# Kernel optimization log

Hardware: AMD Instinct MI355X
Metric: run time of the kernel (lower is better)

## Reference

```python
import jax, jax.numpy as jnp
import numpy as np

N, E, QL, HID = 1024, 8192, 8, 1024
NH, NKV, HD = 16, 8, 64          # heads, kv heads, head_dim; groups = NH // NKV = 2
INTER = 4096
THETA = 10000.0
EPS = 1e-6


def rmsnorm(x, w):
    v = x.astype(jnp.float32)
    v = v * jax.lax.rsqrt(jnp.mean(v * v, axis=-1, keepdims=True) + EPS)
    return w * v.astype(x.dtype)


def rotate_half(x):
    h = x.shape[-1] // 2
    return jnp.concatenate([-x[..., h:], x[..., :h]], axis=-1)


def rope_tables(seq_len):
    inv_freq = 1.0 / (THETA ** (jnp.arange(0, HD, 2, dtype=jnp.float32) / HD))
    freqs = jnp.arange(seq_len, dtype=jnp.float32)[:, None] * inv_freq[None, :]
    emb = jnp.concatenate([freqs, freqs], axis=-1)  # [seq_len, HD]
    return jnp.cos(emb), jnp.sin(emb)


def setup_inputs() -> dict:
    key = jax.random.key(0)
    ks = jax.random.split(key, 14)
    w = lambda k, sh: (jax.random.normal(k, sh, jnp.float32) * 0.02)
    return {
        "hidden_states": jax.random.normal(ks[0], (N, QL, HID), jnp.float32),
        "edge_index": jax.random.randint(ks[1], (2, E), 0, N, dtype=jnp.int32),
        "edge_hidden_states": jax.random.normal(ks[2], (E, QL, HID), jnp.float32),
        "Wq": w(ks[3], (NH * HD, HID)),
        "Wk": w(ks[4], (NKV * HD, HID)),
        "Wv": w(ks[5], (NKV * HD, HID)),
        "Wo": w(ks[6], (HID, HID)),
        "Wgate": w(ks[7], (INTER, HID)),
        "Wup": w(ks[8], (INTER, HID)),
        "Wdown": w(ks[9], (HID, INTER)),
        "ln1_w": jnp.ones((HID,), jnp.float32),
        "ln2_w": jnp.ones((HID,), jnp.float32),
    }


def gofa_layer(hidden_states, edge_index, edge_hidden_states, Wq, Wk, Wv, Wo,
               Wgate, Wup, Wdown, ln1_w, ln2_w):
    src, dst = edge_index[0], edge_index[1]  # message flows src -> dst
    residual = hidden_states
    x = rmsnorm(hidden_states, ln1_w)  # [N, QL, HID]

    q = x @ Wq.T                     # [N, QL, NH*HD]
    k = x @ Wk.T                     # [N, QL, NKV*HD]
    v = x @ Wv.T
    ek = edge_hidden_states @ Wk.T   # [E, QL, NKV*HD]
    ev = edge_hidden_states @ Wv.T

    # per-edge gather
    q_i = q[dst]                     # [E, QL, NH*HD]
    k_j, v_j = k[src], v[src]        # [E, QL, NKV*HD]

    # interleave node/edge tokens: [E, 2*QL, NKV*HD]
    keys = jnp.stack([k_j, ek], axis=2).reshape(E, 2 * QL, NKV * HD)
    vals = jnp.stack([v_j, ev], axis=2).reshape(E, 2 * QL, NKV * HD)

    qh = q_i.reshape(E, QL, NH, HD).transpose(0, 2, 1, 3)        # [E, NH, QL, HD]
    kh = keys.reshape(E, 2 * QL, NKV, HD).transpose(0, 2, 1, 3)  # [E, NKV, 2QL, HD]
    vh = vals.reshape(E, 2 * QL, NKV, HD).transpose(0, 2, 1, 3)

    cos_k, sin_k = rope_tables(2 * QL)
    cos_q, sin_q = cos_k[:QL], sin_k[:QL]
    qh = qh * cos_q[None, None] + rotate_half(qh) * sin_q[None, None]
    kh = kh * cos_k[None, None] + rotate_half(kh) * sin_k[None, None]

    groups = NH // NKV
    kh = jnp.repeat(kh, groups, axis=1)  # [E, NH, 2QL, HD]
    vh = jnp.repeat(vh, groups, axis=1)

    logits = jnp.einsum('ehqd,ehkd->ehqk', qh, kh) / np.sqrt(HD)  # [E, NH, QL, 2QL]

    # segment softmax over (edges into same dst node) x (2QL key positions)
    seg = jnp.repeat(dst, 2 * QL)                                  # [E*2QL]
    a = logits.transpose(0, 3, 1, 2).reshape(E * 2 * QL, NH, QL)   # [E*2QL, NH, QL]
    m = jax.ops.segment_max(a, seg, num_segments=N)                # [N, NH, QL]
    ex = jnp.exp(a - m[seg])
    s = jax.ops.segment_sum(ex, seg, num_segments=N)
    alpha = ex / (s[seg] + 1e-16)
    alpha = alpha.reshape(E, 2 * QL, NH, QL).transpose(0, 2, 3, 1)  # [E, NH, QL, 2QL]

    out_e = jnp.einsum('ehqk,ehkd->ehqd', alpha, vh)               # [E, NH, QL, HD]
    out_e = out_e.transpose(0, 2, 1, 3).reshape(E, QL, HID)

    agg = jax.ops.segment_sum(out_e, dst, num_segments=N)          # [N, QL, HID]
    attn_out = agg @ Wo.T

    h = residual + attn_out
    h2 = rmsnorm(h, ln2_w)
    mlp = (jax.nn.silu(h2 @ Wgate.T) * (h2 @ Wup.T)) @ Wdown.T
    return h + mlp


def reference(hidden_states, edge_index, edge_hidden_states, Wq, Wk, Wv, Wo,
              Wgate, Wup, Wdown, ln1_w, ln2_w):
    return gofa_layer(hidden_states, edge_index, edge_hidden_states, Wq, Wk, Wv,
                      Wo, Wgate, Wup, Wdown, ln1_w, ln2_w)
```

## Files before the change

### kernel.cpp

```cpp
#include <hip/hip_runtime.h>
#include <cstddef>
#include <cstdint>

constexpr int kN    = 1024;
constexpr int kE    = 8192;
constexpr int kQL   = 8;
constexpr int kHID  = 1024;

typedef __bf16 bf16x8 __attribute__((ext_vector_type(8)));
typedef float  f32x4  __attribute__((ext_vector_type(4)));
typedef unsigned short ushort8 __attribute__((ext_vector_type(8)));

__device__ __forceinline__ unsigned short f2bf(float f) {
  unsigned u = __float_as_uint(f);
  unsigned r = (u + 0x7FFFu + ((u >> 16) & 1u)) >> 16;
  return (unsigned short)r;
}
__device__ __forceinline__ float bf2f(unsigned short u) {
  return __uint_as_float((unsigned)u << 16);
}
__device__ __forceinline__ unsigned pkbf(float a, float b) {
  return (unsigned)f2bf(a) | ((unsigned)f2bf(b) << 16);
}
__device__ __forceinline__ void gload_lds16(const void* g, void* l) {
  __builtin_amdgcn_global_load_lds(
      (const __attribute__((address_space(1))) void*)g,
      (__attribute__((address_space(3))) void*)l, 16, 0, 0);
}

__global__ void rope_tables_kernel(float* __restrict__ ct, float* __restrict__ st) {
  int i = threadIdx.x;
  int p = i >> 5, j = i & 31;
  float inv = expf(-((float)(2 * j) / 64.0f) * logf(10000.0f));
  float ang = (float)p * inv;
  ct[i] = cosf(ang);
  st[i] = sinf(ang);
}

__global__ __launch_bounds__(256) void cvt_kernel(
    const float* __restrict__ in, unsigned short* __restrict__ out, int n8) {
  int i = blockIdx.x * 256 + threadIdx.x;
  if (i >= n8) return;
  const float4* p = (const float4*)(in + (size_t)i * 8);
  float4 a = p[0], b = p[1];
  uint4 o;
  o.x = f2bf(a.x) | ((unsigned)f2bf(a.y) << 16);
  o.y = f2bf(a.z) | ((unsigned)f2bf(a.w) << 16);
  o.z = f2bf(b.x) | ((unsigned)f2bf(b.y) << 16);
  o.w = f2bf(b.z) | ((unsigned)f2bf(b.w) << 16);
  *(uint4*)(out + (size_t)i * 8) = o;
}

__global__ __launch_bounds__(256) void cvt_gu_kernel(
    const float* __restrict__ Wg, const float* __restrict__ Wu,
    unsigned short* __restrict__ out) {
  int i = blockIdx.x * 256 + threadIdx.x;
  int n = i >> 7, ck = (i & 127) * 8;
  int isUp = (n >> 4) & 1;
  int srow = (n >> 6) * 32 + ((n >> 5) & 1) * 16 + (n & 15);
  const float* src = (isUp ? Wu : Wg) + (size_t)srow * 1024 + ck;
  const float4* p = (const float4*)src;
  float4 a = p[0], b = p[1];
  uint4 o;
  o.x = f2bf(a.x) | ((unsigned)f2bf(a.y) << 16);
  o.y = f2bf(a.z) | ((unsigned)f2bf(a.w) << 16);
  o.z = f2bf(b.x) | ((unsigned)f2bf(b.y) << 16);
  o.w = f2bf(b.z) | ((unsigned)f2bf(b.w) << 16);
  *(uint4*)(out + (size_t)n * 1024 + ck) = o;
}

__global__ __launch_bounds__(256) void rmsnorm_bf16_kernel(
    const float* __restrict__ in, const float* __restrict__ w,
    unsigned short* __restrict__ out) {
  __shared__ float red[4];
  int row = blockIdx.x, tid = threadIdx.x;
  const float* p = in + (size_t)row * kHID + tid * 4;
  float4 v = *(const float4*)p;
  float ss = v.x*v.x + v.y*v.y + v.z*v.z + v.w*v.w;
  #pragma unroll
  for (int off = 32; off > 0; off >>= 1) ss += __shfl_down(ss, off);
  int lane = tid & 63, wv = tid >> 6;
  if (lane == 0) red[wv] = ss;
  __syncthreads();
  float tot = red[0] + red[1] + red[2] + red[3];
  float rn = rsqrtf(tot * (1.0f / (float)kHID) + 1e-6f);
  float4 w4 = *(const float4*)(w + tid * 4);
  uint2 o;
  o.x = f2bf(v.x*rn*w4.x) | ((unsigned)f2bf(v.y*rn*w4.y) << 16);
  o.y = f2bf(v.z*rn*w4.z) | ((unsigned)f2bf(v.w*rn*w4.w) << 16);
  *(uint2*)(out + (size_t)row * kHID + tid * 4) = o;
}

template<int OUTMODE, int TM>
__global__ __launch_bounds__(512, 4) void gemmk(
    const unsigned short* __restrict__ A, const unsigned short* __restrict__ B,
    const float* __restrict__ resid, void* __restrict__ Cout,
    const float* __restrict__ ct, const float* __restrict__ st,
    int M, int N, int K) {
  constexpr int ABUFE = TM * 32;
  constexpr int BBUFE = 128 * 32;
  constexpr int WRS   = TM / 4;
  constexpr int MI    = WRS / 16;
  constexpr int LPS   = (TM == 256) ? 3 : 2;
  __shared__ unsigned short As[3 * ABUFE];
  __shared__ unsigned short Bs[3 * BBUFE];
  const int tid = threadIdx.x;
  const int lane = tid & 63, wid = tid >> 6;
  const int gx = gridDim.x;
  int id = blockIdx.y * gx + blockIdx.x;
  {
    const int nwg = gx * gridDim.y;
    const int cpx = nwg >> 3;
    id = (id & 7) * cpx + (id >> 3);
  }
  const int m0 = (id / gx) * TM, n0 = (id % gx) * 128;
  const int wr = wid >> 1, wc = wid & 1;
  const int l15 = lane & 15, lg = lane >> 4;
  const int NT = K >> 5;

  const int sr4 = lane >> 2, sc = lane & 3;
  const int arow0 = (TM == 256) ? (wid * 32 + sr4) : (wid * 16 + sr4);
  const int brow0 = wid * 16 + sr4;
  const unsigned short* Asrc = A + (size_t)(m0 + arow0) * K + (sc ^ ((arow0 >> 1) & 3)) * 8;
  const unsigned short* Bsrc = B + (size_t)(n0 + brow0) * K + (sc ^ ((brow0 >> 1) & 3)) * 8;
  const size_t rK16 = (size_t)16 * K;

#define STAGE(t_, b_) do {                                                   \
    const size_t _k0 = (size_t)(t_) * 32;                                    \
    if (TM == 256) {                                                         \
      gload_lds16(Asrc + _k0,        As + (b_) * ABUFE + wid * 1024);        \
      gload_lds16(Asrc + rK16 + _k0, As + (b_) * ABUFE + wid * 1024 + 512);  \
    } else {                                                                 \
      gload_lds16(Asrc + _k0,        As + (b_) * ABUFE + wid * 512);         \
    }                                                                        \
    gload_lds16(Bsrc + _k0,          Bs + (b_) * BBUFE + wid * 512);         \
  } while (0)

  f32x4 acc[MI][4] = {};
  STAGE(0, 0); STAGE(1, 1);

  const int rck = (lg ^ ((l15 >> 1) & 3)) * 8;
  int cur = 0, nx2 = 2;
  for (int t = 0; t < NT; ++t) {
    __builtin_amdgcn_sched_barrier(0);
    if (t + 1 < NT) asm volatile("s_waitcnt vmcnt(%0)" :: "i"(LPS) : "memory");
    else            asm volatile("s_waitcnt vmcnt(0)" ::: "memory");
    __builtin_amdgcn_s_barrier();
    __builtin_amdgcn_sched_barrier(0);
    if (t + 2 < NT) STAGE(t + 2, nx2);

    const unsigned short* Ab = As + cur * ABUFE + (wr * WRS + l15) * 32 + rck;
    const unsigned short* Bb = Bs + cur * BBUFE + (wc * 64 + l15) * 32 + rck;
    bf16x8 af[MI], bf[4];
    #pragma unroll
    for (int mi = 0; mi < MI; ++mi) af[mi] = *(const bf16x8*)(Ab + mi * 512);
    #pragma unroll
    for (int nj = 0; nj < 4; ++nj) bf[nj] = *(const bf16x8*)(Bb + nj * 512);
    __builtin_amdgcn_s_setprio(1);
    #pragma unroll
    for (int mi = 0; mi < MI; ++mi)
      #pragma unroll
      for (int nj = 0; nj < 4; ++nj)
        acc[mi][nj] = __builtin_amdgcn_mfma_f32_16x16x32_bf16(af[mi], bf[nj], acc[mi][nj], 0, 0, 0);
    __builtin_amdgcn_s_setprio(0);
    cur = (cur == 2) ? 0 : cur + 1;
    nx2 = (nx2 == 2) ? 0 : nx2 + 1;
  }
#undef STAGE

  const int r0 = lg * 4;
  const int bc = n0 + wc * 64;
  #pragma unroll
  for (int mi = 0; mi < MI; ++mi) {
    #pragma unroll
    for (int r = 0; r < 4; ++r) {
      const size_t grow = (size_t)(m0 + wr * WRS + mi * 16 + r0 + r);
      if (OUTMODE == 0) {
        #pragma unroll
        for (int nj = 0; nj < 4; ++nj) {
          const size_t gi = grow * N + (bc + nj * 16 + l15);
          float v = acc[mi][nj][r];
          if (resid) v += resid[gi];
          ((float*)Cout)[gi] = v;
        }
      } else if (OUTMODE == 2) {
        #pragma unroll
        for (int p = 0; p < 2; ++p) {
          float gv = acc[mi][2 * p][r], uv = acc[mi][2 * p + 1][r];
          float res = gv / (1.f + __expf(-gv)) * uv;
          ((unsigned short*)Cout)[grow * (size_t)(N >> 1) + (bc >> 1) + p * 16 + l15] = f2bf(res);
        }
      } else {
        bool doR = false; int pos = 0;
        if (OUTMODE == 3) { doR = bc < 512; pos = 2 * ((int)grow & 7) + 1; }
        if (OUTMODE == 4) {
          if (bc < 1024)      { doR = true; pos = (int)grow & 7; }
          else if (bc < 1536) { doR = true; pos = 2 * ((int)grow & 7); }
        }
        unsigned short* o16 = (unsigned short*)Cout;
        if (doR) {
          #pragma unroll
          for (int nj = 0; nj < 2; ++nj) {
            float a = acc[mi][nj][r], b = acc[mi][nj + 2][r];
            float c = ct[pos * 32 + nj * 16 + l15];
            float s = st[pos * 32 + nj * 16 + l15];
            o16[grow * N + bc + nj * 16 + l15]       = f2bf(a * c - b * s);
            o16[grow * N + bc + (nj + 2) * 16 + l15] = f2bf(b * c + a * s);
          }
        } else {
          #pragma unroll
          for (int nj = 0; nj < 4; ++nj)
            o16[grow * N + bc + nj * 16 + l15] = f2bf(acc[mi][nj][r]);
        }
      }
    }
  }
}

__global__ void csr_count_kernel(const int* __restrict__ dst, int* __restrict__ cnt) {
  int e = blockIdx.x * 256 + threadIdx.x;
  if (e < kE) atomicAdd(&cnt[dst[e]], 1);
}
__global__ __launch_bounds__(1024) void csr_scan_kernel(
    const int* __restrict__ cnt, int* __restrict__ start) {
  __shared__ int tmp[1024];
  int t = threadIdx.x;
  tmp[t] = cnt[t];
  __syncthreads();
  for (int off = 1; off < 1024; off <<= 1) {
    int add = (t >= off) ? tmp[t - off] : 0;
    __syncthreads();
    tmp[t] += add;
    __syncthreads();
  }
  start[t + 1] = tmp[t];
  if (t == 0) start[0] = 0;
}
__global__ void csr_scatter_kernel(const int* __restrict__ dst, const int* __restrict__ start,
                                   int* __restrict__ cursor, int* __restrict__ elist) {
  int e = blockIdx.x * 256 + threadIdx.x;
  if (e < kE) {
    int d = dst[e];
    int pos = atomicAdd(&cursor[d], 1);
    elist[start[d] + pos] = e;
  }
}

__global__ __launch_bounds__(256) void attn_mfma_kernel(
    const unsigned short* __restrict__ qkv,
    const unsigned short* __restrict__ ekv,
    const int* __restrict__ srcIdx, const int* __restrict__ elist,
    const int* __restrict__ start,
    unsigned short* __restrict__ aggb) {
  const int n = blockIdx.x >> 1;
  const int g = (blockIdx.x & 1) * 4 + (threadIdx.x >> 6);
  const int lane = threadIdx.x & 63;
  const int l15 = lane & 15, lg = lane >> 4;

  const int h = g * 2 + (l15 >> 3), q = l15 & 7;
  const unsigned short* qrow = qkv + ((size_t)n * 8 + q) * 2048 + h * 64 + lg * 8;
  const bf16x8 qf0 = *(const bf16x8*)qrow;
  const bf16x8 qf1 = *(const bf16x8*)(qrow + 32);

  float m = -3.4e38f, sh = 0.f;
  f32x4 oacc[4];
  #pragma unroll
  for (int t = 0; t < 4; ++t) oacc[t] = (f32x4){0.f, 0.f, 0.f, 0.f};

  const int kparity = l15 & 1;
  const int t_ = l15 >> 1;
  const int lgh = lg & 1;
  const int eS = lg >> 1;

  const int s0 = start[n], s1 = start[n + 1];
  for (int jj = s0; jj < s1; jj += 2) {
    const int e0 = elist[jj];
    const bool has1 = (jj + 1 < s1);
    const int e1 = has1 ? elist[jj + 1] : e0;
    const int sn0 = srcIdx[e0], sn1 = srcIdx[e1];

    const unsigned short* kr0 = kparity
        ? ekv + ((size_t)e0 * 8 + t_) * 1024 + g * 64 + lg * 8
        : qkv + ((size_t)sn0 * 8 + t_) * 2048 + 1024 + g * 64 + lg * 8;
    const unsigned short* kr1 = kparity
        ? ekv + ((size_t)e1 * 8 + t_) * 1024 + g * 64 + lg * 8
        : qkv + ((size_t)sn1 * 8 + t_) * 2048 + 1024 + g * 64 + lg * 8;
    bf16x8 ka0 = *(const bf16x8*)kr0, ka1 = *(const bf16x8*)(kr0 + 32);
    bf16x8 kc0 = *(const bf16x8*)kr1, kc1 = *(const bf16x8*)(kr1 + 32);

    const int evsel = eS ? e1 : e0;
    const int snsel = eS ? sn1 : sn0;
    const unsigned short* vn = qkv + ((size_t)snsel * 8 + lgh * 4) * 2048 + 1536 + g * 64;
    const unsigned short* ve = ekv + ((size_t)evsel * 8 + lgh * 4) * 1024 + 512 + g * 64;

    f32x4 z = (f32x4){0.f, 0.f, 0.f, 0.f};
    f32x4 sa = __builtin_amdgcn_mfma_f32_16x16x32_bf16(ka0, qf0, z, 0, 0, 0);
    sa       = __builtin_amdgcn_mfma_f32_16x16x32_bf16(ka1, qf1, sa, 0, 0, 0);
    f32x4 sb = __builtin_amdgcn_mfma_f32_16x16x32_bf16(kc0, qf0, z, 0, 0, 0);
    sb       = __builtin_amdgcn_mfma_f32_16x16x32_bf16(kc1, qf1, sb, 0, 0, 0);

    float l0[4], l1[4];
    float lmax = -3.4e38f;
    #pragma unroll
    for (int r = 0; r < 4; ++r) {
      l0[r] = sa[r] * 0.125f;
      l1[r] = has1 ? sb[r] * 0.125f : -3.4e38f;
      lmax = fmaxf(lmax, fmaxf(l0[r], l1[r]));
    }
    lmax = fmaxf(lmax, __shfl_xor(lmax, 16));
    lmax = fmaxf(lmax, __shfl_xor(lmax, 32));
    const float mnew = fmaxf(m, lmax);
    const float scale = __expf(m - mnew);
    float p0[4], p1[4], ps = 0.f;
    #pragma unroll
    for (int r = 0; r < 4; ++r) {
      p0[r] = __expf(l0[r] - mnew);
      p1[r] = __expf(l1[r] - mnew);
      ps += p0[r] + p1[r];
    }
    ps += __shfl_xor(ps, 16);
    ps += __shfl_xor(ps, 32);
    sh = sh * scale + ps;
    m = mnew;

    #pragma unroll
    for (int r = 0; r < 4; ++r) {
      float sr = __shfl(scale, lg * 4 + r);
      #pragma unroll
      for (int t = 0; t < 4; ++t) oacc[t][r] *= sr;
    }

    unsigned w00 = pkbf(p0[0], p0[1]), w01 = pkbf(p0[2], p0[3]);
    unsigned w10 = pkbf(p1[0], p1[1]), w11 = pkbf(p1[2], p1[3]);
    const int L1 = l15 + 32 * lgh, L2 = L1 + 16;
    unsigned a0 = __shfl(w00, L1), a1 = __shfl(w01, L1);
    unsigned a2 = __shfl(w00, L2), a3 = __shfl(w01, L2);
    unsigned b0 = __shfl(w10, L1), b1 = __shfl(w11, L1);
    unsigned b2 = __shfl(w10, L2), b3 = __shfl(w11, L2);
    uint4 wv;
    wv.x = eS ? b0 : a0; wv.y = eS ? b1 : a1;
    wv.z = eS ? b2 : a2; wv.w = eS ? b3 : a3;
    const bf16x8 pf = __builtin_bit_cast(bf16x8, wv);

    #pragma unroll
    for (int t = 0; t < 4; ++t) {
      const int col = t * 16 + l15;
      ushort8 vr;
      #pragma unroll
      for (int j = 0; j < 8; ++j)
        vr[j] = (j & 1) ? ve[(j >> 1) * 1024 + col] : vn[(j >> 1) * 2048 + col];
      const bf16x8 vf = __builtin_bit_cast(bf16x8, vr);
      oacc[t] = __builtin_amdgcn_mfma_f32_16x16x32_bf16(pf, vf, oacc[t], 0, 0, 0);
    }
  }

  #pragma unroll
  for (int r = 0; r < 4; ++r) {
    const float sr = __shfl(sh, lg * 4 + r);
    const float inv = 1.f / (sr + 1e-16f);
    const int hq = lg * 4 + r;
    const int hh = g * 2 + (hq >> 3), qq = hq & 7;
    unsigned short* op = aggb + ((size_t)n * 8 + qq) * 1024 + hh * 64 + l15;
    #pragma unroll
    for (int t = 0; t < 4; ++t) op[t * 16] = f2bf(oacc[t][r] * inv);
  }
}

extern "C" void kernel_launch(void* const* d_in, const int* in_sizes, int n_in,
                              void* d_out, int out_size, void* d_ws, size_t ws_size,
                              hipStream_t stream) {
  const float* hidden = (const float*)d_in[0];
  const int*   eidx   = (const int*)d_in[1];
  const float* ehid   = (const float*)d_in[2];
  const float* Wq     = (const float*)d_in[3];
  const float* Wk     = (const float*)d_in[4];
  const float* Wv     = (const float*)d_in[5];
  const float* Wo     = (const float*)d_in[6];
  const float* Wgate  = (const float*)d_in[7];
  const float* Wup    = (const float*)d_in[8];
  const float* Wdown  = (const float*)d_in[9];
  const float* ln1    = (const float*)d_in[10];
  const float* ln2    = (const float*)d_in[11];
  const int* srcIdx = eidx;
  const int* dstIdx = eidx + kE;

  char* wsb = (char*)d_ws;
  size_t off = 0;
  auto alloc = [&](size_t bytes) { char* p = wsb + off; off += (bytes + 255) & ~(size_t)255; return p; };
  unsigned short* eh16   = (unsigned short*)alloc(134217728);
  unsigned short* ekv16  = (unsigned short*)alloc(134217728);
  unsigned short* qkv16  = (unsigned short*)alloc(33554432);
  unsigned short* x16    = (unsigned short*)alloc(16777216);
  unsigned short* agg16  = (unsigned short*)alloc(16777216);
  float*          hbuf   = (float*)alloc(33554432);
  unsigned short* wqkv16 = (unsigned short*)alloc(4194304);
  unsigned short* wo16   = (unsigned short*)alloc(2097152);
  unsigned short* wgu16  = (unsigned short*)alloc(16777216);
  unsigned short* wd16   = (unsigned short*)alloc(8388608);
  int* cnt    = (int*)alloc(4096);
  int* cursor = (int*)alloc(4096);
  int* startb = (int*)alloc(4352);
  int* elist  = (int*)alloc(32768);
  float* ct   = (float*)alloc(2048);
  float* st   = (float*)alloc(2048);
  unsigned short* gm16 = ekv16;
  unsigned short* h216 = x16;
  float* outp = (float*)d_out;

  hipMemsetAsync(cnt, 0, 8192, stream);
  rope_tables_kernel<<<1, 512, 0, stream>>>(ct, st);

  cvt_kernel<<<32768, 256, 0, stream>>>(ehid,  eh16, 8388608);
  cvt_kernel<<<512,   256, 0, stream>>>(Wq,    wqkv16,                 131072);
  cvt_kernel<<<256,   256, 0, stream>>>(Wk,    wqkv16 + 1024 * 1024,   65536);
  cvt_kernel<<<256,   256, 0, stream>>>(Wv,    wqkv16 + 1536 * 1024,   65536);
  cvt_kernel<<<512,   256, 0, stream>>>(Wo,    wo16,                  131072);
  cvt_gu_kernel<<<4096, 256, 0, stream>>>(Wgate, Wup, wgu16);
  cvt_kernel<<<2048,  256, 0, stream>>>(Wdown, wd16,                  524288);

  csr_count_kernel<<<32, 256, 0, stream>>>(dstIdx, cnt);
  csr_scan_kernel<<<1, 1024, 0, stream>>>(cnt, startb);
  csr_scatter_kernel<<<32, 256, 0, stream>>>(dstIdx, startb, cursor, elist);

  rmsnorm_bf16_kernel<<<kN * kQL, 256, 0, stream>>>(hidden, ln1, x16);

  gemmk<4, 256><<<dim3(16, 32),  512, 0, stream>>>(x16,  wqkv16, nullptr, qkv16, ct, st, 8192, 2048, 1024);
  gemmk<3, 256><<<dim3(8, 256), 512, 0, stream>>>(eh16, wqkv16 + 1024 * 1024, nullptr, ekv16, ct, st, 65536, 1024, 1024);

  attn_mfma_kernel<<<2048, 256, 0, stream>>>(qkv16, ekv16, srcIdx, elist, startb, agg16);

  gemmk<0, 128><<<dim3(8, 64), 512, 0, stream>>>(agg16, wo16, hidden, hbuf, ct, st, 8192, 1024, 1024);

  rmsnorm_bf16_kernel<<<kN * kQL, 256, 0, stream>>>(hbuf, ln2, h216);
  gemmk<2, 256><<<dim3(64, 32), 512, 0, stream>>>(h216, wgu16, nullptr, gm16, ct, st, 8192, 8192, 1024);
  gemmk<0, 128><<<dim3(8, 64), 512, 0, stream>>>(gm16, wd16, hbuf, outp, ct, st, 8192, 1024, 4096);
}
```

Measured before the change: 708.0 us.

## Fuse fp32-to-bf16 edge conversion into edge KV GEMM and simplify GEMM pipeline

Removes the standalone conversion of the large fp32 edge hidden-state tensor to bf16. A new GEMM variant instead loads fp32 A tiles into registers, converts them, and writes them to LDS while prefetching the next tile. All GEMMs also switch from a 512-thread, triple-buffered, 256-row-tile kernel to a simpler 256-thread, single-buffered 128x128 kernel with two syncthreads per k-step. This saves a full write and re-read of the edge bf16 buffer, but gives up the asynchronous multi-stage pipelining in every GEMM.

```diff
diff --git a/kernel.cpp b/kernel.cpp
--- a/kernel.cpp
+++ b/kernel.cpp
@@ -91,19 +91,14 @@
   *(uint2*)(out + (size_t)row * kHID + tid * 4) = o;
 }
 
-template<int OUTMODE, int TM>
-__global__ __launch_bounds__(512, 4) void gemmk(
+template<int OUTMODE>
+__global__ __launch_bounds__(256) void gemm97(
     const unsigned short* __restrict__ A, const unsigned short* __restrict__ B,
     const float* __restrict__ resid, void* __restrict__ Cout,
     const float* __restrict__ ct, const float* __restrict__ st,
     int M, int N, int K) {
-  constexpr int ABUFE = TM * 32;
-  constexpr int BBUFE = 128 * 32;
-  constexpr int WRS   = TM / 4;
-  constexpr int MI    = WRS / 16;
-  constexpr int LPS   = (TM == 256) ? 3 : 2;
-  __shared__ unsigned short As[3 * ABUFE];
-  __shared__ unsigned short Bs[3 * BBUFE];
+  __shared__ unsigned short As[4096];
+  __shared__ unsigned short Bs[4096];
   const int tid = threadIdx.x;
   const int lane = tid & 63, wid = tid >> 6;
   const int gx = gridDim.x;
@@ -113,68 +108,47 @@
     const int cpx = nwg >> 3;
     id = (id & 7) * cpx + (id >> 3);
   }
-  const int m0 = (id / gx) * TM, n0 = (id % gx) * 128;
+  const int m0 = (id / gx) * 128, n0 = (id % gx) * 128;
   const int wr = wid >> 1, wc = wid & 1;
   const int l15 = lane & 15, lg = lane >> 4;
   const int NT = K >> 5;
 
-  const int sr4 = lane >> 2, sc = lane & 3;
-  const int arow0 = (TM == 256) ? (wid * 32 + sr4) : (wid * 16 + sr4);
-  const int brow0 = wid * 16 + sr4;
-  const unsigned short* Asrc = A + (size_t)(m0 + arow0) * K + (sc ^ ((arow0 >> 1) & 3)) * 8;
-  const unsigned short* Bsrc = B + (size_t)(n0 + brow0) * K + (sc ^ ((brow0 >> 1) & 3)) * 8;
-  const size_t rK16 = (size_t)16 * K;
-
-#define STAGE(t_, b_) do {                                                   \
-    const size_t _k0 = (size_t)(t_) * 32;                                    \
-    if (TM == 256) {                                                         \
-      gload_lds16(Asrc + _k0,        As + (b_) * ABUFE + wid * 1024);        \
-      gload_lds16(Asrc + rK16 + _k0, As + (b_) * ABUFE + wid * 1024 + 512);  \
-    } else {                                                                 \
-      gload_lds16(Asrc + _k0,        As + (b_) * ABUFE + wid * 512);         \
-    }                                                                        \
-    gload_lds16(Bsrc + _k0,          Bs + (b_) * BBUFE + wid * 512);         \
-  } while (0)
-
-  f32x4 acc[MI][4] = {};
-  STAGE(0, 0); STAGE(1, 1);
-
+  const int sr = tid >> 2, sc = tid & 3;
+  const unsigned short* Asrc = A + (size_t)(m0 + sr) * K + (sc ^ ((sr >> 1) & 3)) * 8;
+  const unsigned short* Bsrc = B + (size_t)(n0 + sr) * K + (sc ^ ((sr >> 1) & 3)) * 8;
+  const size_t rK64 = (size_t)64 * K;
   const int rck = (lg ^ ((l15 >> 1) & 3)) * 8;
-  int cur = 0, nx2 = 2;
+
+  f32x4 acc[4][4] = {};
   for (int t = 0; t < NT; ++t) {
-    __builtin_amdgcn_sched_barrier(0);
-    if (t + 1 < NT) asm volatile("s_waitcnt vmcnt(%0)" :: "i"(LPS) : "memory");
-    else            asm volatile("s_waitcnt vmcnt(0)" ::: "memory");
-    __builtin_amdgcn_s_barrier();
-    __builtin_amdgcn_sched_barrier(0);
-    if (t + 2 < NT) STAGE(t + 2, nx2);
-
-    const unsigned short* Ab = As + cur * ABUFE + (wr * WRS + l15) * 32 + rck;
-    const unsigned short* Bb = Bs + cur * BBUFE + (wc * 64 + l15) * 32 + rck;
-    bf16x8 af[MI], bf[4];
-    #pragma unroll
-    for (int mi = 0; mi < MI; ++mi) af[mi] = *(const bf16x8*)(Ab + mi * 512);
-    #pragma unroll
-    for (int nj = 0; nj < 4; ++nj) bf[nj] = *(const bf16x8*)(Bb + nj * 512);
-    __builtin_amdgcn_s_setprio(1);
-    #pragma unroll
-    for (int mi = 0; mi < MI; ++mi)
+    __syncthreads();
+    const size_t k0 = (size_t)t * 32;
+    gload_lds16(Asrc + k0,        As + wid * 512);
+    gload_lds16(Asrc + rK64 + k0, As + 2048 + wid * 512);
+    gload_lds16(Bsrc + k0,        Bs + wid * 512);
+    gload_lds16(Bsrc + rK64 + k0, Bs + 2048 + wid * 512);
+    __syncthreads();
+    bf16x8 af[4], bf[4];
+    #pragma unroll
+    for (int mi = 0; mi < 4; ++mi)
+      af[mi] = *(const bf16x8*)&As[(wr * 64 + mi * 16 + l15) * 32 + rck];
+    #pragma unroll
+    for (int nj = 0; nj < 4; ++nj)
+      bf[nj] = *(const bf16x8*)&Bs[(wc * 64 + nj * 16 + l15) * 32 + rck];
+    #pragma unroll
+    for (int mi = 0; mi < 4; ++mi)
       #pragma unroll
       for (int nj = 0; nj < 4; ++nj)
         acc[mi][nj] = __builtin_amdgcn_mfma_f32_16x16x32_bf16(af[mi], bf[nj], acc[mi][nj], 0, 0, 0);
-    __builtin_amdgcn_s_setprio(0);
-    cur = (cur == 2) ? 0 : cur + 1;
-    nx2 = (nx2 == 2) ? 0 : nx2 + 1;
-  }
-#undef STAGE
+  }
 
   const int r0 = lg * 4;
   const int bc = n0 + wc * 64;
   #pragma unroll
-  for (int mi = 0; mi < MI; ++mi) {
+  for (int mi = 0; mi < 4; ++mi) {
     #pragma unroll
     for (int r = 0; r < 4; ++r) {
-      const size_t grow = (size_t)(m0 + wr * WRS + mi * 16 + r0 + r);
+      const size_t grow = (size_t)(m0 + wr * 64 + mi * 16 + r0 + r);
       if (OUTMODE == 0) {
         #pragma unroll
         for (int nj = 0; nj < 4; ++nj) {
@@ -192,11 +166,8 @@
         }
       } else {
         bool doR = false; int pos = 0;
-        if (OUTMODE == 3) { doR = bc < 512; pos = 2 * ((int)grow & 7) + 1; }
-        if (OUTMODE == 4) {
-          if (bc < 1024)      { doR = true; pos = (int)grow & 7; }
-          else if (bc < 1536) { doR = true; pos = 2 * ((int)grow & 7); }
-        }
+        if (bc < 1024)      { doR = true; pos = (int)grow & 7; }
+        else if (bc < 1536) { doR = true; pos = 2 * ((int)grow & 7); }
         unsigned short* o16 = (unsigned short*)Cout;
         if (doR) {
           #pragma unroll
@@ -212,6 +183,102 @@
           for (int nj = 0; nj < 4; ++nj)
             o16[grow * N + bc + nj * 16 + l15] = f2bf(acc[mi][nj][r]);
         }
+      }
+    }
+  }
+}
+
+__global__ __launch_bounds__(256) void gemm97f(
+    const float* __restrict__ Af, const unsigned short* __restrict__ B,
+    unsigned short* __restrict__ Cout,
+    const float* __restrict__ ct, const float* __restrict__ st,
+    int M, int N, int K) {
+  __shared__ unsigned short As[4096];
+  __shared__ unsigned short Bs[4096];
+  const int tid = threadIdx.x;
+  const int lane = tid & 63, wid = tid >> 6;
+  const int gx = gridDim.x;
+  int id = blockIdx.y * gx + blockIdx.x;
+  {
+    const int nwg = gx * gridDim.y;
+    const int cpx = nwg >> 3;
+    id = (id & 7) * cpx + (id >> 3);
+  }
+  const int m0 = (id / gx) * 128, n0 = (id % gx) * 128;
+  const int wr = wid >> 1, wc = wid & 1;
+  const int l15 = lane & 15, lg = lane >> 4;
+  const int NT = K >> 5;
+
+  const int sr = tid >> 2, sc = tid & 3;
+  const int cx = sc ^ ((sr >> 1) & 3);
+  const float* arow0 = Af + (size_t)(m0 + sr) * K + sc * 8;
+  const float* arow1 = arow0 + (size_t)64 * K;
+  unsigned short* dw0 = As + sr * 32 + cx * 8;
+  unsigned short* dw1 = dw0 + 2048;
+  const unsigned short* Bsrc = B + (size_t)(n0 + sr) * K + cx * 8;
+  const size_t rK64 = (size_t)64 * K;
+  const int rck = (lg ^ ((l15 >> 1) & 3)) * 8;
+
+  f32x4 a00, a01, a10, a11;
+  { const float* p = arow0; a00 = *(const f32x4*)p; a01 = *(const f32x4*)(p + 4);
+    const float* q = arow1; a10 = *(const f32x4*)q; a11 = *(const f32x4*)(q + 4); }
+
+  f32x4 acc[4][4] = {};
+  for (int t = 0; t < NT; ++t) {
+    __syncthreads();
+    ushort8 w0, w1;
+    #pragma unroll
+    for (int z = 0; z < 4; ++z) {
+      w0[z] = f2bf(a00[z]); w0[z + 4] = f2bf(a01[z]);
+      w1[z] = f2bf(a10[z]); w1[z + 4] = f2bf(a11[z]);
+    }
+    *(ushort8*)dw0 = w0;
+    *(ushort8*)dw1 = w1;
+    const size_t k0 = (size_t)t * 32;
+    gload_lds16(Bsrc + k0,        Bs + wid * 512);
+    gload_lds16(Bsrc + rK64 + k0, Bs + 2048 + wid * 512);
+    __syncthreads();
+    if (t + 1 < NT) {
+      const float* p = arow0 + (size_t)(t + 1) * 32;
+      const float* q = arow1 + (size_t)(t + 1) * 32;
+      a00 = *(const f32x4*)p; a01 = *(const f32x4*)(p + 4);
+      a10 = *(const f32x4*)q; a11 = *(const f32x4*)(q + 4);
+    }
+    bf16x8 af[4], bf[4];
+    #pragma unroll
+    for (int mi = 0; mi < 4; ++mi)
+      af[mi] = *(const bf16x8*)&As[(wr * 64 + mi * 16 + l15) * 32 + rck];
+    #pragma unroll
+    for (int nj = 0; nj < 4; ++nj)
+      bf[nj] = *(const bf16x8*)&Bs[(wc * 64 + nj * 16 + l15) * 32 + rck];
+    #pragma unroll
+    for (int mi = 0; mi < 4; ++mi)
+      #pragma unroll
+      for (int nj = 0; nj < 4; ++nj)
+        acc[mi][nj] = __builtin_amdgcn_mfma_f32_16x16x32_bf16(af[mi], bf[nj], acc[mi][nj], 0, 0, 0);
+  }
+
+  const int r0 = lg * 4;
+  const int bc = n0 + wc * 64;
+  #pragma unroll
+  for (int mi = 0; mi < 4; ++mi) {
+    #pragma unroll
+    for (int r = 0; r < 4; ++r) {
+      const size_t grow = (size_t)(m0 + wr * 64 + mi * 16 + r0 + r);
+      if (bc < 512) {
+        const int pos = 2 * ((int)grow & 7) + 1;
+        #pragma unroll
+        for (int nj = 0; nj < 2; ++nj) {
+          float a = acc[mi][nj][r], b = acc[mi][nj + 2][r];
+          float c = ct[pos * 32 + nj * 16 + l15];
+          float s = st[pos * 32 + nj * 16 + l15];
+          Cout[grow * N + bc + nj * 16 + l15]       = f2bf(a * c - b * s);
+          Cout[grow * N + bc + (nj + 2) * 16 + l15] = f2bf(b * c + a * s);
+        }
+      } else {
+        #pragma unroll
+        for (int nj = 0; nj < 4; ++nj)
+          Cout[grow * N + bc + nj * 16 + l15] = f2bf(acc[mi][nj][r]);
       }
     }
   }
@@ -387,7 +454,6 @@
   char* wsb = (char*)d_ws;
   size_t off = 0;
   auto alloc = [&](size_t bytes) { char* p = wsb + off; off += (bytes + 255) & ~(size_t)255; return p; };
-  unsigned short* eh16   = (unsigned short*)alloc(134217728);
   unsigned short* ekv16  = (unsigned short*)alloc(134217728);
   unsigned short* qkv16  = (unsigned short*)alloc(33554432);
   unsigned short* x16    = (unsigned short*)alloc(16777216);
@@ -410,7 +476,6 @@
   hipMemsetAsync(cnt, 0, 8192, stream);
   rope_tables_kernel<<<1, 512, 0, stream>>>(ct, st);
 
-  cvt_kernel<<<32768, 256, 0, stream>>>(ehid,  eh16, 8388608);
   cvt_kernel<<<512,   256, 0, stream>>>(Wq,    wqkv16,                 131072);
   cvt_kernel<<<256,   256, 0, stream>>>(Wk,    wqkv16 + 1024 * 1024,   65536);
   cvt_kernel<<<256,   256, 0, stream>>>(Wv,    wqkv16 + 1536 * 1024,   65536);
@@ -424,14 +489,14 @@
 
   rmsnorm_bf16_kernel<<<kN * kQL, 256, 0, stream>>>(hidden, ln1, x16);
 
-  gemmk<4, 256><<<dim3(16, 32),  512, 0, stream>>>(x16,  wqkv16, nullptr, qkv16, ct, st, 8192, 2048, 1024);
-  gemmk<3, 256><<<dim3(8, 256), 512, 0, stream>>>(eh16, wqkv16 + 1024 * 1024, nullptr, ekv16, ct, st, 65536, 1024, 1024);
+  gemm97<4><<<dim3(16, 64), 256, 0, stream>>>(x16, wqkv16, nullptr, qkv16, ct, st, 8192, 2048, 1024);
+  gemm97f<<<dim3(8, 512), 256, 0, stream>>>(ehid, wqkv16 + 1024 * 1024, ekv16, ct, st, 65536, 1024, 1024);
 
   attn_mfma_kernel<<<2048, 256, 0, stream>>>(qkv16, ekv16, srcIdx, elist, startb, agg16);
 
-  gemmk<0, 128><<<dim3(8, 64), 512, 0, stream>>>(agg16, wo16, hidden, hbuf, ct, st, 8192, 1024, 1024);
+  gemm97<0><<<dim3(8, 64), 256, 0, stream>>>(agg16, wo16, hidden, hbuf, ct, st, 8192, 1024, 1024);
 
   rmsnorm_bf16_kernel<<<kN * kQL, 256, 0, stream>>>(hbuf, ln2, h216);
-  gemmk<2, 256><<<dim3(64, 32), 512, 0, stream>>>(h216, wgu16, nullptr, gm16, ct, st, 8192, 8192, 1024);
-  gemmk<0, 128><<<dim3(8, 64), 512, 0, stream>>>(gm16, wd16, hbuf, outp, ct, st, 8192, 1024, 4096);
-}
+  gemm97<2><<<dim3(64, 64), 256, 0, stream>>>(h216, wgu16, nullptr, gm16, ct, st, 8192, 8192, 1024);
+  gemm97<0><<<dim3(8, 64), 256, 0, stream>>>(gm16, wd16, hbuf, outp, ct, st, 8192, 1024, 4096);
+}
```

Result: slower. 816.2 us (+15.3%).

## Restructure GEMM to four waves with larger per-wave output tiles

Applied to the files above, without the earlier changes.

The bf16 MFMA GEMM kernel drops from 512 to 256 threads per block while keeping the same block tile. Each wave now covers twice as many output rows (WRS = TM/2), so the accumulator array doubles. Global-to-LDS staging is rewritten as loops over 64-row chunks, and the launch-bounds occupancy hints and vmcnt waits are adjusted to match. The aim is more fragment reuse per wave and fewer waves contending for LDS and barriers, at the cost of higher register pressure and less latency hiding from wave-level parallelism.

```diff
diff --git a/kernel.cpp b/kernel.cpp
--- a/kernel.cpp
+++ b/kernel.cpp
@@ -92,16 +92,17 @@
 }
 
 template<int OUTMODE, int TM>
-__global__ __launch_bounds__(512, 4) void gemmk(
+__global__ __launch_bounds__(256, (TM == 256) ? 2 : 3) void gemmw(
     const unsigned short* __restrict__ A, const unsigned short* __restrict__ B,
     const float* __restrict__ resid, void* __restrict__ Cout,
     const float* __restrict__ ct, const float* __restrict__ st,
     int M, int N, int K) {
   constexpr int ABUFE = TM * 32;
   constexpr int BBUFE = 128 * 32;
-  constexpr int WRS   = TM / 4;
+  constexpr int WRS   = TM / 2;
   constexpr int MI    = WRS / 16;
-  constexpr int LPS   = (TM == 256) ? 3 : 2;
+  constexpr int AR    = TM / 64;
+  constexpr int LPS   = AR + 2;
   __shared__ unsigned short As[3 * ABUFE];
   __shared__ unsigned short Bs[3 * BBUFE];
   const int tid = threadIdx.x;
@@ -118,22 +119,21 @@
   const int l15 = lane & 15, lg = lane >> 4;
   const int NT = K >> 5;
 
-  const int sr4 = lane >> 2, sc = lane & 3;
-  const int arow0 = (TM == 256) ? (wid * 32 + sr4) : (wid * 16 + sr4);
-  const int brow0 = wid * 16 + sr4;
-  const unsigned short* Asrc = A + (size_t)(m0 + arow0) * K + (sc ^ ((arow0 >> 1) & 3)) * 8;
-  const unsigned short* Bsrc = B + (size_t)(n0 + brow0) * K + (sc ^ ((brow0 >> 1) & 3)) * 8;
-  const size_t rK16 = (size_t)16 * K;
+  const int sr = tid >> 2, sc = tid & 3;
+  const unsigned short* Asrc = A + (size_t)(m0 + sr) * K + (sc ^ ((sr >> 1) & 3)) * 8;
+  const unsigned short* Bsrc = B + (size_t)(n0 + sr) * K + (sc ^ ((sr >> 1) & 3)) * 8;
+  const size_t rK64 = (size_t)64 * K;
 
 #define STAGE(t_, b_) do {                                                   \
     const size_t _k0 = (size_t)(t_) * 32;                                    \
-    if (TM == 256) {                                                         \
-      gload_lds16(Asrc + _k0,        As + (b_) * ABUFE + wid * 1024);        \
-      gload_lds16(Asrc + rK16 + _k0, As + (b_) * ABUFE + wid * 1024 + 512);  \
-    } else {                                                                 \
-      gload_lds16(Asrc + _k0,        As + (b_) * ABUFE + wid * 512);         \
-    }                                                                        \
-    gload_lds16(Bsrc + _k0,          Bs + (b_) * BBUFE + wid * 512);         \
+    _Pragma("unroll")                                                        \
+    for (int rr = 0; rr < AR; ++rr)                                          \
+      gload_lds16(Asrc + rr * rK64 + _k0,                                    \
+                  As + (b_) * ABUFE + (wid * 16 + rr * 64) * 32);            \
+    _Pragma("unroll")                                                        \
+    for (int rr = 0; rr < 2; ++rr)                                           \
+      gload_lds16(Bsrc + rr * rK64 + _k0,                                    \
+                  Bs + (b_) * BBUFE + (wid * 16 + rr * 64) * 32);            \
   } while (0)
 
   f32x4 acc[MI][4] = {};
@@ -424,14 +424,14 @@
 
   rmsnorm_bf16_kernel<<<kN * kQL, 256, 0, stream>>>(hidden, ln1, x16);
 
-  gemmk<4, 256><<<dim3(16, 32),  512, 0, stream>>>(x16,  wqkv16, nullptr, qkv16, ct, st, 8192, 2048, 1024);
-  gemmk<3, 256><<<dim3(8, 256), 512, 0, stream>>>(eh16, wqkv16 + 1024 * 1024, nullptr, ekv16, ct, st, 65536, 1024, 1024);
+  gemmw<4, 256><<<dim3(16, 32), 256, 0, stream>>>(x16,  wqkv16, nullptr, qkv16, ct, st, 8192, 2048, 1024);
+  gemmw<3, 256><<<dim3(8, 256), 256, 0, stream>>>(eh16, wqkv16 + 1024 * 1024, nullptr, ekv16, ct, st, 65536, 1024, 1024);
 
   attn_mfma_kernel<<<2048, 256, 0, stream>>>(qkv16, ekv16, srcIdx, elist, startb, agg16);
 
-  gemmk<0, 128><<<dim3(8, 64), 512, 0, stream>>>(agg16, wo16, hidden, hbuf, ct, st, 8192, 1024, 1024);
+  gemmw<0, 128><<<dim3(8, 64), 256, 0, stream>>>(agg16, wo16, hidden, hbuf, ct, st, 8192, 1024, 1024);
 
   rmsnorm_bf16_kernel<<<kN * kQL, 256, 0, stream>>>(hbuf, ln2, h216);
-  gemmk<2, 256><<<dim3(64, 32), 512, 0, stream>>>(h216, wgu16, nullptr, gm16, ct, st, 8192, 8192, 1024);
-  gemmk<0, 128><<<dim3(8, 64), 512, 0, stream>>>(gm16, wd16, hbuf, outp, ct, st, 8192, 1024, 4096);
-}
+  gemmw<2, 256><<<dim3(64, 32), 256, 0, stream>>>(h216, wgu16, nullptr, gm16, ct, st, 8192, 8192, 1024);
+  gemmw<0, 128><<<dim3(8, 64), 256, 0, stream>>>(gm16, wd16, hbuf, outp, ct, st, 8192, 1024, 4096);
+}
```

Measured after the change: 749.5 us. +5.9%, slower.
